# Performance work log

Measured on AMD Instinct MI355X. Metric: run time of the kernel, lower is better.

## Reference

```python
import jax, jax.numpy as jnp
import numpy as np

B, S, D, H = 4, 2048, 1024, 16
DK = D // H

def setup_inputs() -> dict:
    key = jax.random.key(0)
    ks = jax.random.split(key, 13)
    std = 1.0 / np.sqrt(D)
    inp = {
        'query': jax.random.normal(ks[0], (B, S, D), jnp.float32),
        'key':   jax.random.normal(ks[1], (B, S, D), jnp.float32),
        'value': jax.random.normal(ks[2], (B, S, D), jnp.float32),
        'mask':  jax.random.randint(ks[3], (B, 1, S), 0, 2, jnp.int32),
        'Wq': jax.random.normal(ks[4], (D, D), jnp.float32) * std,
        'bq': jnp.zeros((D,), jnp.float32),
        'Wk': jax.random.normal(ks[5], (D, D), jnp.float32) * std,
        'bk': jnp.zeros((D,), jnp.float32),
        'Wv': jax.random.normal(ks[6], (D, D), jnp.float32) * std,
        'bv': jnp.zeros((D,), jnp.float32),
        'Wo': jax.random.normal(ks[7], (D, D), jnp.float32) * std,
        'bo': jnp.zeros((D,), jnp.float32),
    }
    return inp

def reference(query, key, value, mask, Wq, bq, Wk, bk, Wv, bv, Wo, bo):
    # QKV projections (torch Linear: x @ W.T + b), reshape to [B,H,S,DK]
    def proj(x, W, b):
        y = x @ W.T + b
        return y.reshape(B, S, H, DK).transpose(0, 2, 1, 3)
    q = proj(query, Wq, bq)
    k = proj(key, Wk, bk)
    v = proj(value, Wv, bv)
    scores = jnp.einsum('bhqd,bhkd->bhqk', q, k) / jnp.sqrt(jnp.float32(DK))
    # mask [B,1,S] -> unsqueeze head dim -> [B,1,1,S], broadcast over h,q
    m = mask[:, None, :, :]  # [B,1,1,S]
    scores = jnp.where(m == 0, jnp.float32(-1e9), scores)
    p = jax.nn.softmax(scores, axis=-1)  # dropout omitted (eval mode)
    x = jnp.einsum('bhqk,bhkd->bhqd', p, v)
    x = x.transpose(0, 2, 1, 3).reshape(B, S, D)
    return x @ Wo.T + bo
```

## Files before the change

kernel.cpp:

```cpp
#include <hip/hip_runtime.h>

typedef unsigned short u16;
typedef __bf16 bf16x8 __attribute__((ext_vector_type(8)));
typedef float f32x4 __attribute__((ext_vector_type(4)));
typedef u16 u16x8 __attribute__((ext_vector_type(8)));
typedef u16 u16x4 __attribute__((ext_vector_type(4)));

typedef __attribute__((address_space(1))) const unsigned char gc_u8;
typedef __attribute__((address_space(3))) unsigned char lds_u8;

__device__ inline void gload16(const void* g, void* l) {
    __builtin_amdgcn_global_load_lds((gc_u8*)g, (lds_u8*)l, 16, 0, 0);
}
__device__ inline u16 f2bf(float f) {
    union { __bf16 h; u16 u; } c; c.h = (__bf16)f; return c.u;
}
__device__ inline float bf2f(u16 u) {
    union { u16 u[2]; float f; } c; c.u[0] = 0; c.u[1] = u; return c.f;
}
__device__ inline void hard_barrier() {
    __builtin_amdgcn_sched_barrier(0);
    __builtin_amdgcn_s_barrier();
    __builtin_amdgcn_sched_barrier(0);
}
#define WAIT_LGKM0() asm volatile("s_waitcnt lgkmcnt(0)" ::: "memory")
#define WAIT_VMCNT(n) asm volatile("s_waitcnt vmcnt(" #n ")" ::: "memory")

__global__ __launch_bounds__(256) void cvt4(const float* __restrict__ s0,
                                            const float* __restrict__ s1,
                                            const float* __restrict__ s2,
                                            const float* __restrict__ s3,
                                            u16* __restrict__ d0, u16* __restrict__ d1,
                                            u16* __restrict__ d2, u16* __restrict__ d3,
                                            int n) {
    const int y = blockIdx.y;
    const float* src = (y == 0) ? s0 : (y == 1) ? s1 : (y == 2) ? s2 : s3;
    u16* dst = (y == 0) ? d0 : (y == 1) ? d1 : (y == 2) ? d2 : d3;
    int i = (blockIdx.x * 256 + threadIdx.x) * 4;
    if (i < n) {
        float4 f = *reinterpret_cast<const float4*>(src + i);
        u16x4 u = { f2bf(f.x), f2bf(f.y), f2bf(f.z), f2bf(f.w) };
        *reinterpret_cast<u16x4*>(dst + i) = u;
    }
}
__global__ __launch_bounds__(256) void cvt3(const float* __restrict__ s0,
                                            const float* __restrict__ s1,
                                            const float* __restrict__ s2,
                                            u16* __restrict__ d0, u16* __restrict__ d1,
                                            u16* __restrict__ d2, int n) {
    const int y = blockIdx.y;
    const float* src = (y == 0) ? s0 : (y == 1) ? s1 : s2;
    u16* dst = (y == 0) ? d0 : (y == 1) ? d1 : d2;
    int i = (blockIdx.x * 256 + threadIdx.x) * 4;
    if (i < n) {
        float4 f = *reinterpret_cast<const float4*>(src + i);
        u16x4 u = { f2bf(f.x), f2bf(f.y), f2bf(f.z), f2bf(f.w) };
        *reinterpret_cast<u16x4*>(dst + i) = u;
    }
}

__global__ __launch_bounds__(256) void gemm_qkv(const u16* __restrict__ Aq,
                                                const u16* __restrict__ Ak,
                                                const u16* __restrict__ Av,
                                                const u16* __restrict__ Bq,
                                                const u16* __restrict__ Bk,
                                                const u16* __restrict__ Bv,
                                                const float* __restrict__ bq,
                                                const float* __restrict__ bk,
                                                const float* __restrict__ bv,
                                                u16* __restrict__ Cq,
                                                u16* __restrict__ Ck,
                                                u16* __restrict__ Cvp,
                                                int M, int N, int K) {
    __shared__ __align__(16) u16 As[2][128][32];
    __shared__ __align__(16) u16 Bs[2][128][32];
    const int z = blockIdx.z;
    const u16* A = (z == 0) ? Aq : (z == 1) ? Ak : Av;
    const u16* B = (z == 0) ? Bq : (z == 1) ? Bk : Bv;
    const float* bias = (z == 0) ? bq : (z == 1) ? bk : bv;
    u16* Cv = (z == 0) ? Cq : (z == 1) ? Ck : Cvp;
    const bool vmode = (z == 2);

    const int t = threadIdx.x, lane = t & 63, w = t >> 6;
    const int wr = w >> 1, wc = w & 1;
    const int l15 = lane & 15, l16 = lane >> 4;
    const int nwg = gridDim.x, ntiles = N >> 7;
    const int wg = blockIdx.x, chunk = nwg >> 3;
    const int swz = (wg & 7) * chunk + (wg >> 3);
    const int bm = (swz / ntiles) * 128, bn = (swz % ntiles) * 128;
    const int srow = w * 16 + (lane >> 2);
    const int sgr = (lane & 3) * 8;
    const u16* Ab = A + (size_t)bm * K;
    const u16* Bb = B + (size_t)bn * K;

    f32x4 acc[4][4];
#pragma unroll
    for (int i = 0; i < 4; i++)
#pragma unroll
        for (int j = 0; j < 4; j++) acc[i][j] = (f32x4){0.f, 0.f, 0.f, 0.f};

    auto stage = [&](int c, int k0) {
        gload16(Ab + (size_t)srow * K + k0 + sgr,        &As[c][w * 16][0]);
        gload16(Ab + (size_t)(64 + srow) * K + k0 + sgr, &As[c][64 + w * 16][0]);
        gload16(Bb + (size_t)srow * K + k0 + sgr,        &Bs[c][w * 16][0]);
        gload16(Bb + (size_t)(64 + srow) * K + k0 + sgr, &Bs[c][64 + w * 16][0]);
    };

    stage(0, 0);
    __syncthreads();

    const int NS = K >> 5;
    for (int i = 0; i < NS; ++i) {
        const int c = i & 1;
        WAIT_LGKM0();
        hard_barrier();
        if (i + 1 < NS) {
            stage(c ^ 1, (i + 1) * 32);
            WAIT_VMCNT(4);
        } else {
            WAIT_VMCNT(0);
        }
        hard_barrier();

        bf16x8 afr[4], bfr[4];
#pragma unroll
        for (int mi = 0; mi < 4; mi++)
            afr[mi] = *(const bf16x8*)&As[c][wr * 64 + mi * 16 + l15][l16 * 8];
#pragma unroll
        for (int ni = 0; ni < 4; ni++)
            bfr[ni] = *(const bf16x8*)&Bs[c][wc * 64 + ni * 16 + l15][l16 * 8];
#pragma unroll
        for (int mi = 0; mi < 4; mi++)
#pragma unroll
            for (int ni = 0; ni < 4; ni++)
                acc[mi][ni] = __builtin_amdgcn_mfma_f32_16x16x32_bf16(
                    afr[mi], bfr[ni], acc[mi][ni], 0, 0, 0);
    }

#pragma unroll
    for (int ni = 0; ni < 4; ni++) {
        const int col = bn + wc * 64 + ni * 16 + l15;
        const float bv2 = bias[col];
#pragma unroll
        for (int mi = 0; mi < 4; mi++) {
            const int r0 = bm + wr * 64 + mi * 16 + l16 * 4;
            if (vmode) {
                const int bb = r0 >> 11, ss = r0 & 2047;
                const int hh = col >> 6, dk = col & 63;
                u16x4 pk;
#pragma unroll
                for (int r = 0; r < 4; r++) pk[r] = f2bf(acc[mi][ni][r] + bv2);
                *(u16x4*)&Cv[(((size_t)(bb * 16 + hh) * 64 + dk) << 11) + ss] = pk;
            } else {
#pragma unroll
                for (int r = 0; r < 4; r++)
                    Cv[(size_t)(r0 + r) * N + col] = f2bf(acc[mi][ni][r] + bv2);
            }
        }
    }
}

__global__ __launch_bounds__(256) void gemm_out(const u16* __restrict__ A,
                                                const u16* __restrict__ B,
                                                const float* __restrict__ bias,
                                                float* __restrict__ Cv,
                                                int M, int N, int K) {
    __shared__ __align__(16) u16 As[2][128][32];
    __shared__ __align__(16) u16 Bs[2][128][32];
    const int t = threadIdx.x, lane = t & 63, w = t >> 6;
    const int wr = w >> 1, wc = w & 1;
    const int l15 = lane & 15, l16 = lane >> 4;
    const int nwg = gridDim.x, ntiles = N >> 7;
    const int wg = blockIdx.x, chunk = nwg >> 3;
    const int swz = (wg & 7) * chunk + (wg >> 3);
    const int bm = (swz / ntiles) * 128, bn = (swz % ntiles) * 128;
    const int srow = w * 16 + (lane >> 2);
    const int sgr = (lane & 3) * 8;
    const u16* Ab = A + (size_t)bm * K;
    const u16* Bb = B + (size_t)bn * K;

    f32x4 acc[4][4];
#pragma unroll
    for (int i = 0; i < 4; i++)
#pragma unroll
        for (int j = 0; j < 4; j++) acc[i][j] = (f32x4){0.f, 0.f, 0.f, 0.f};

    auto stage = [&](int c, int k0) {
        gload16(Ab + (size_t)srow * K + k0 + sgr,        &As[c][w * 16][0]);
        gload16(Ab + (size_t)(64 + srow) * K + k0 + sgr, &As[c][64 + w * 16][0]);
        gload16(Bb + (size_t)srow * K + k0 + sgr,        &Bs[c][w * 16][0]);
        gload16(Bb + (size_t)(64 + srow) * K + k0 + sgr, &Bs[c][64 + w * 16][0]);
    };

    stage(0, 0);
    __syncthreads();

    const int NS = K >> 5;
    for (int i = 0; i < NS; ++i) {
        const int c = i & 1;
        WAIT_LGKM0();
        hard_barrier();
        if (i + 1 < NS) {
            stage(c ^ 1, (i + 1) * 32);
            WAIT_VMCNT(4);
        } else {
            WAIT_VMCNT(0);
        }
        hard_barrier();

        bf16x8 afr[4], bfr[4];
#pragma unroll
        for (int mi = 0; mi < 4; mi++)
            afr[mi] = *(const bf16x8*)&As[c][wr * 64 + mi * 16 + l15][l16 * 8];
#pragma unroll
        for (int ni = 0; ni < 4; ni++)
            bfr[ni] = *(const bf16x8*)&Bs[c][wc * 64 + ni * 16 + l15][l16 * 8];
#pragma unroll
        for (int mi = 0; mi < 4; mi++)
#pragma unroll
            for (int ni = 0; ni < 4; ni++)
                acc[mi][ni] = __builtin_amdgcn_mfma_f32_16x16x32_bf16(
                    afr[mi], bfr[ni], acc[mi][ni], 0, 0, 0);
    }

#pragma unroll
    for (int ni = 0; ni < 4; ni++) {
        const int col = bn + wc * 64 + ni * 16 + l15;
        const float bv = bias[col];
#pragma unroll
        for (int mi = 0; mi < 4; mi++) {
            const int r0 = bm + wr * 64 + mi * 16 + l16 * 4;
#pragma unroll
            for (int r = 0; r < 4; r++)
                Cv[(size_t)(r0 + r) * N + col] = acc[mi][ni][r] + bv;
        }
    }
}

__global__ __launch_bounds__(256, 2) void attn_fwd(const u16* __restrict__ Q,
                                                   const u16* __restrict__ Kg,
                                                   const u16* __restrict__ Vt,
                                                   const int* __restrict__ mask,
                                                   u16* __restrict__ O) {
    constexpr int S = 2048, D = 1024;
    __shared__ __align__(16) u16 Kl[2][2][2][64][32];
    __shared__ __align__(16) u16 Vl[2][2][2][64][32];
    __shared__ __align__(16) u16 Pl[4][16][68];
    __shared__ unsigned Mb[64];
    const int t = threadIdx.x, lane = t & 63, w = t >> 6;
    const int l15 = lane & 15, l16 = lane >> 4;
    const int wg = blockIdx.x;
    const int swz = (wg & 7) * 64 + (wg >> 3);
    const int q0 = (swz & 7) * 256, h = (swz >> 3) & 15, b = swz >> 7;
    const int qb = q0 + w * 64;
    const int srow = w * 16 + (lane >> 2);
    const int sgr = ((lane & 3) ^ ((lane >> 3) & 3)) * 8;
    const int gsw8 = (l16 ^ ((l15 >> 1) & 3)) * 8;

    const u16* Khead = Kg + (size_t)b * S * D + h * 64;
    const u16* Vthead = Vt + (size_t)(b * 16 + h) * 64 * 2048;
    const int* mrow = mask + b * S;

    auto stage = [&](int c, int kt) {
#pragma unroll
        for (int kg = 0; kg < 2; kg++) {
            const int k0 = kt + kg * 64;
            gload16(Khead + (size_t)(k0 + srow) * D + sgr,        &Kl[c][kg][0][w * 16][0]);
            gload16(Khead + (size_t)(k0 + srow) * D + 32 + sgr,   &Kl[c][kg][1][w * 16][0]);
            gload16(Vthead + (size_t)srow * 2048 + k0 + sgr,      &Vl[c][kg][0][w * 16][0]);
            gload16(Vthead + (size_t)srow * 2048 + k0 + 32 + sgr, &Vl[c][kg][1][w * 16][0]);
        }
    };

    stage(0, 0);
#pragma unroll
    for (int j = 0; j < 8; j++) {
        unsigned long long bal = __ballot(mrow[j * 256 + w * 64 + lane] != 0);
        if (lane == 0) {
            Mb[(j * 4 + w) * 2]     = (unsigned)bal;
            Mb[(j * 4 + w) * 2 + 1] = (unsigned)(bal >> 32);
        }
    }

    constexpr float QSCALE = 0.125f * 1.44269504f;
    bf16x8 aq[4][2];
#pragma unroll
    for (int qt = 0; qt < 4; qt++)
#pragma unroll
        for (int ks = 0; ks < 2; ks++) {
            const size_t qi = ((size_t)b * S + qb + qt * 16 + l15) * D +
                              h * 64 + ks * 32 + l16 * 8;
            u16x8 raw = *(const u16x8*)&Q[qi];
            bf16x8 qv;
#pragma unroll
            for (int i = 0; i < 8; i++) qv[i] = (__bf16)(bf2f(raw[i]) * QSCALE);
            aq[qt][ks] = qv;
        }

    bf16x8 ones;
#pragma unroll
    for (int i = 0; i < 8; i++) ones[i] = (__bf16)1.0f;

    f32x4 acc[4][4];
    f32x4 accl[4];
#pragma unroll
    for (int qt = 0; qt < 4; qt++) {
        accl[qt] = (f32x4){0.f, 0.f, 0.f, 0.f};
#pragma unroll
        for (int dt = 0; dt < 4; dt++) acc[qt][dt] = (f32x4){0.f, 0.f, 0.f, 0.f};
    }

    __syncthreads();

    for (int tile = 0; tile < S / 128; ++tile) {
        const int c = tile & 1;
        const int cur = tile * 128;
        WAIT_LGKM0();
        hard_barrier();
        if (tile + 1 < S / 128) {
            stage(c ^ 1, cur + 128);
            WAIT_VMCNT(8);
        } else {
            WAIT_VMCNT(0);
        }
        hard_barrier();

#pragma unroll
        for (int kg = 0; kg < 2; kg++) {
            bf16x8 kf0[4], kf1[4], vf0[4], vf1[4];
#pragma unroll
            for (int k4 = 0; k4 < 4; k4++) {
                kf0[k4] = *(const bf16x8*)&Kl[c][kg][0][k4 * 16 + l15][gsw8];
                kf1[k4] = *(const bf16x8*)&Kl[c][kg][1][k4 * 16 + l15][gsw8];
            }
#pragma unroll
            for (int dt = 0; dt < 4; dt++) {
                vf0[dt] = *(const bf16x8*)&Vl[c][kg][0][dt * 16 + l15][gsw8];
                vf1[dt] = *(const bf16x8*)&Vl[c][kg][1][dt * 16 + l15][gsw8];
            }

            const int mb0 = (cur >> 5) + kg * 2;
            const unsigned w0 = Mb[mb0], w1 = Mb[mb0 + 1];
            float madd[4][4];
#pragma unroll
            for (int k4 = 0; k4 < 4; k4++) {
                const unsigned wsel = (k4 < 2) ? w0 : w1;
                const unsigned bits = (wsel >> ((k4 & 1) * 16 + l16 * 4)) & 0xFu;
#pragma unroll
                for (int r = 0; r < 4; r++)
                    madd[k4][r] = ((bits >> r) & 1u) ? 0.f : -1.0e9f;
            }

#pragma unroll
            for (int qt = 0; qt < 4; qt++) {
#pragma unroll
                for (int k4 = 0; k4 < 4; k4++) {
                    f32x4 z = (f32x4){0.f, 0.f, 0.f, 0.f};
                    z = __builtin_amdgcn_mfma_f32_16x16x32_bf16(kf0[k4], aq[qt][0], z, 0, 0, 0);
                    z = __builtin_amdgcn_mfma_f32_16x16x32_bf16(kf1[k4], aq[qt][1], z, 0, 0, 0);
                    u16x4 pk;
#pragma unroll
                    for (int r = 0; r < 4; r++)
                        pk[r] = f2bf(__builtin_amdgcn_exp2f(z[r] + madd[k4][r]));
                    *(u16x4*)&Pl[w][l15][k4 * 16 + l16 * 4] = pk;
                }
                bf16x8 pa0 = *(const bf16x8*)&Pl[w][l15][l16 * 8];
                bf16x8 pa1 = *(const bf16x8*)&Pl[w][l15][32 + l16 * 8];
                accl[qt] = __builtin_amdgcn_mfma_f32_16x16x32_bf16(pa0, ones, accl[qt], 0, 0, 0);
                accl[qt] = __builtin_amdgcn_mfma_f32_16x16x32_bf16(pa1, ones, accl[qt], 0, 0, 0);
#pragma unroll
                for (int dt = 0; dt < 4; dt++) {
                    acc[qt][dt] = __builtin_amdgcn_mfma_f32_16x16x32_bf16(
                        pa0, vf0[dt], acc[qt][dt], 0, 0, 0);
                    acc[qt][dt] = __builtin_amdgcn_mfma_f32_16x16x32_bf16(
                        pa1, vf1[dt], acc[qt][dt], 0, 0, 0);
                }
            }
        }
    }

#pragma unroll
    for (int qt = 0; qt < 4; qt++) {
        f32x4 inv;
#pragma unroll
        for (int r = 0; r < 4; r++) inv[r] = 1.f / accl[qt][r];
#pragma unroll
        for (int dt = 0; dt < 4; dt++)
#pragma unroll
            for (int r = 0; r < 4; r++) {
                const int tok = qb + qt * 16 + l16 * 4 + r;
                O[((size_t)b * S + tok) * D + h * 64 + dt * 16 + l15] =
                    f2bf(acc[qt][dt][r] * inv[r]);
            }
    }
}

extern "C" void kernel_launch(void* const* d_in, const int* in_sizes, int n_in,
                              void* d_out, int out_size, void* d_ws, size_t ws_size,
                              hipStream_t stream) {
    const float* query = (const float*)d_in[0];
    const float* key   = (const float*)d_in[1];
    const float* value = (const float*)d_in[2];
    const int*   mask  = (const int*)d_in[3];
    const float* Wq = (const float*)d_in[4];
    const float* bq = (const float*)d_in[5];
    const float* Wk = (const float*)d_in[6];
    const float* bk = (const float*)d_in[7];
    const float* Wv = (const float*)d_in[8];
    const float* bv = (const float*)d_in[9];
    const float* Wo = (const float*)d_in[10];
    const float* bo = (const float*)d_in[11];
    float* out = (float*)d_out;

    constexpr int S = 2048, D = 1024;
    constexpr size_t MSZ = (size_t)4 * S * D;
    constexpr size_t WSZ = (size_t)D * D;
    const size_t need = 4 * WSZ * 2 + 4 * MSZ * 2;
    if (ws_size < need) return;

    char* p = (char*)d_ws;
    u16* Wqb = (u16*)p; p += WSZ * 2;
    u16* Wkb = (u16*)p; p += WSZ * 2;
    u16* Wvb = (u16*)p; p += WSZ * 2;
    u16* Wob = (u16*)p; p += WSZ * 2;
    u16* Aq  = (u16*)p; p += MSZ * 2;
    u16* Qb  = (u16*)p; p += MSZ * 2;
    u16* Kb  = (u16*)p; p += MSZ * 2;
    u16* Vtb = (u16*)p; p += MSZ * 2;
    u16* Ak = (u16*)d_out;
    u16* Av = (u16*)d_out + MSZ;
    u16* Xb = Aq;

    cvt4<<<dim3(WSZ / 1024, 4), 256, 0, stream>>>(Wq, Wk, Wv, Wo,
                                                  Wqb, Wkb, Wvb, Wob, (int)WSZ);
    cvt3<<<dim3(MSZ / 1024, 3), 256, 0, stream>>>(query, key, value,
                                                  Aq, Ak, Av, (int)MSZ);
    gemm_qkv<<<dim3(512, 1, 3), 256, 0, stream>>>(Aq, Ak, Av, Wqb, Wkb, Wvb,
                                                  bq, bk, bv, Qb, Kb, Vtb,
                                                  8192, 1024, 1024);
    attn_fwd<<<512, 256, 0, stream>>>(Qb, Kb, Vtb, mask, Xb);
    gemm_out<<<512, 256, 0, stream>>>(Xb, Wob, bo, out, 8192, 1024, 1024);
}
```

Baseline: 206.5 us.

## Shrink attention blocks to two waves with 64-key tiles and MFMA priority hints

The attention kernel moves from 256-thread blocks covering 256 queries to 128-thread blocks covering 128 queries, launching 1024 blocks instead of 512. The key tile drops from 128 to 64 per iteration, so shared-memory buffers shrink and there are twice as many loop iterations and barriers. The QK scores for all four key sub-tiles are now computed before the exp, and s_setprio hints are placed around the MFMA sections to interleave waves. The aim is more resident blocks and better overlap, at the price of more barrier overhead and each K/V tile being reused by fewer waves.

```diff
diff --git a/kernel.cpp b/kernel.cpp
--- a/kernel.cpp
+++ b/kernel.cpp
@@ -237,21 +237,21 @@
     }
 }
 
-__global__ __launch_bounds__(256, 2) void attn_fwd(const u16* __restrict__ Q,
+__global__ __launch_bounds__(128, 2) void attn_fwd(const u16* __restrict__ Q,
                                                    const u16* __restrict__ Kg,
                                                    const u16* __restrict__ Vt,
                                                    const int* __restrict__ mask,
                                                    u16* __restrict__ O) {
     constexpr int S = 2048, D = 1024;
-    __shared__ __align__(16) u16 Kl[2][2][2][64][32];
-    __shared__ __align__(16) u16 Vl[2][2][2][64][32];
-    __shared__ __align__(16) u16 Pl[4][16][68];
+    __shared__ __align__(16) u16 Kl[2][2][64][32];
+    __shared__ __align__(16) u16 Vl[2][2][64][32];
+    __shared__ __align__(16) u16 Pl[2][16][68];
     __shared__ unsigned Mb[64];
     const int t = threadIdx.x, lane = t & 63, w = t >> 6;
     const int l15 = lane & 15, l16 = lane >> 4;
     const int wg = blockIdx.x;
-    const int swz = (wg & 7) * 64 + (wg >> 3);
-    const int q0 = (swz & 7) * 256, h = (swz >> 3) & 15, b = swz >> 7;
+    const int swz = (wg & 7) * 128 + (wg >> 3);
+    const int q0 = (swz & 15) * 128, h = (swz >> 4) & 15, b = swz >> 8;
     const int qb = q0 + w * 64;
     const int srow = w * 16 + (lane >> 2);
     const int sgr = ((lane & 3) ^ ((lane >> 3) & 3)) * 8;
@@ -262,23 +262,23 @@
     const int* mrow = mask + b * S;
 
     auto stage = [&](int c, int kt) {
-#pragma unroll
-        for (int kg = 0; kg < 2; kg++) {
-            const int k0 = kt + kg * 64;
-            gload16(Khead + (size_t)(k0 + srow) * D + sgr,        &Kl[c][kg][0][w * 16][0]);
-            gload16(Khead + (size_t)(k0 + srow) * D + 32 + sgr,   &Kl[c][kg][1][w * 16][0]);
-            gload16(Vthead + (size_t)srow * 2048 + k0 + sgr,      &Vl[c][kg][0][w * 16][0]);
-            gload16(Vthead + (size_t)srow * 2048 + k0 + 32 + sgr, &Vl[c][kg][1][w * 16][0]);
-        }
+        gload16(Khead + (size_t)(kt + srow) * D + sgr,            &Kl[c][0][w * 16][0]);
+        gload16(Khead + (size_t)(kt + 32 + srow) * D + sgr,       &Kl[c][0][32 + w * 16][0]);
+        gload16(Khead + (size_t)(kt + srow) * D + 32 + sgr,       &Kl[c][1][w * 16][0]);
+        gload16(Khead + (size_t)(kt + 32 + srow) * D + 32 + sgr,  &Kl[c][1][32 + w * 16][0]);
+        gload16(Vthead + (size_t)srow * 2048 + kt + sgr,          &Vl[c][0][w * 16][0]);
+        gload16(Vthead + (size_t)(32 + srow) * 2048 + kt + sgr,   &Vl[c][0][32 + w * 16][0]);
+        gload16(Vthead + (size_t)srow * 2048 + kt + 32 + sgr,     &Vl[c][1][w * 16][0]);
+        gload16(Vthead + (size_t)(32 + srow) * 2048 + kt + 32 + sgr, &Vl[c][1][32 + w * 16][0]);
     };
 
     stage(0, 0);
 #pragma unroll
-    for (int j = 0; j < 8; j++) {
-        unsigned long long bal = __ballot(mrow[j * 256 + w * 64 + lane] != 0);
+    for (int j = 0; j < 16; j++) {
+        unsigned long long bal = __ballot(mrow[j * 128 + w * 64 + lane] != 0);
         if (lane == 0) {
-            Mb[(j * 4 + w) * 2]     = (unsigned)bal;
-            Mb[(j * 4 + w) * 2 + 1] = (unsigned)(bal >> 32);
+            Mb[(j * 2 + w) * 2]     = (unsigned)bal;
+            Mb[(j * 2 + w) * 2 + 1] = (unsigned)(bal >> 32);
         }
     }
 
@@ -312,70 +312,74 @@
 
     __syncthreads();
 
-    for (int tile = 0; tile < S / 128; ++tile) {
+    for (int tile = 0; tile < S / 64; ++tile) {
         const int c = tile & 1;
-        const int cur = tile * 128;
+        const int cur = tile * 64;
         WAIT_LGKM0();
         hard_barrier();
-        if (tile + 1 < S / 128) {
-            stage(c ^ 1, cur + 128);
+        if (tile + 1 < S / 64) {
+            stage(c ^ 1, cur + 64);
             WAIT_VMCNT(8);
         } else {
             WAIT_VMCNT(0);
         }
         hard_barrier();
 
-#pragma unroll
-        for (int kg = 0; kg < 2; kg++) {
-            bf16x8 kf0[4], kf1[4], vf0[4], vf1[4];
+        bf16x8 kf0[4], kf1[4], vf0[4], vf1[4];
+#pragma unroll
+        for (int k4 = 0; k4 < 4; k4++) {
+            kf0[k4] = *(const bf16x8*)&Kl[c][0][k4 * 16 + l15][gsw8];
+            kf1[k4] = *(const bf16x8*)&Kl[c][1][k4 * 16 + l15][gsw8];
+        }
+#pragma unroll
+        for (int dt = 0; dt < 4; dt++) {
+            vf0[dt] = *(const bf16x8*)&Vl[c][0][dt * 16 + l15][gsw8];
+            vf1[dt] = *(const bf16x8*)&Vl[c][1][dt * 16 + l15][gsw8];
+        }
+
+        const unsigned w0 = Mb[cur >> 5], w1 = Mb[(cur >> 5) + 1];
+        float madd[4][4];
+#pragma unroll
+        for (int k4 = 0; k4 < 4; k4++) {
+            const unsigned wsel = (k4 < 2) ? w0 : w1;
+            const unsigned bits = (wsel >> ((k4 & 1) * 16 + l16 * 4)) & 0xFu;
+#pragma unroll
+            for (int r = 0; r < 4; r++)
+                madd[k4][r] = ((bits >> r) & 1u) ? 0.f : -1.0e9f;
+        }
+
+#pragma unroll
+        for (int qt = 0; qt < 4; qt++) {
+            __builtin_amdgcn_s_setprio(1);
+            f32x4 z[4];
 #pragma unroll
             for (int k4 = 0; k4 < 4; k4++) {
-                kf0[k4] = *(const bf16x8*)&Kl[c][kg][0][k4 * 16 + l15][gsw8];
-                kf1[k4] = *(const bf16x8*)&Kl[c][kg][1][k4 * 16 + l15][gsw8];
+                z[k4] = (f32x4){0.f, 0.f, 0.f, 0.f};
+                z[k4] = __builtin_amdgcn_mfma_f32_16x16x32_bf16(kf0[k4], aq[qt][0], z[k4], 0, 0, 0);
+                z[k4] = __builtin_amdgcn_mfma_f32_16x16x32_bf16(kf1[k4], aq[qt][1], z[k4], 0, 0, 0);
             }
+            __builtin_amdgcn_s_setprio(0);
+#pragma unroll
+            for (int k4 = 0; k4 < 4; k4++) {
+                u16x4 pk;
+#pragma unroll
+                for (int r = 0; r < 4; r++)
+                    pk[r] = f2bf(__builtin_amdgcn_exp2f(z[k4][r] + madd[k4][r]));
+                *(u16x4*)&Pl[w][l15][k4 * 16 + l16 * 4] = pk;
+            }
+            bf16x8 pa0 = *(const bf16x8*)&Pl[w][l15][l16 * 8];
+            bf16x8 pa1 = *(const bf16x8*)&Pl[w][l15][32 + l16 * 8];
+            __builtin_amdgcn_s_setprio(1);
+            accl[qt] = __builtin_amdgcn_mfma_f32_16x16x32_bf16(pa0, ones, accl[qt], 0, 0, 0);
+            accl[qt] = __builtin_amdgcn_mfma_f32_16x16x32_bf16(pa1, ones, accl[qt], 0, 0, 0);
 #pragma unroll
             for (int dt = 0; dt < 4; dt++) {
-                vf0[dt] = *(const bf16x8*)&Vl[c][kg][0][dt * 16 + l15][gsw8];
-                vf1[dt] = *(const bf16x8*)&Vl[c][kg][1][dt * 16 + l15][gsw8];
+                acc[qt][dt] = __builtin_amdgcn_mfma_f32_16x16x32_bf16(
+                    pa0, vf0[dt], acc[qt][dt], 0, 0, 0);
+                acc[qt][dt] = __builtin_amdgcn_mfma_f32_16x16x32_bf16(
+                    pa1, vf1[dt], acc[qt][dt], 0, 0, 0);
             }
-
-            const int mb0 = (cur >> 5) + kg * 2;
-            const unsigned w0 = Mb[mb0], w1 = Mb[mb0 + 1];
-            float madd[4][4];
-#pragma unroll
-            for (int k4 = 0; k4 < 4; k4++) {
-                const unsigned wsel = (k4 < 2) ? w0 : w1;
-                const unsigned bits = (wsel >> ((k4 & 1) * 16 + l16 * 4)) & 0xFu;
-#pragma unroll
-                for (int r = 0; r < 4; r++)
-                    madd[k4][r] = ((bits >> r) & 1u) ? 0.f : -1.0e9f;
-            }
-
-#pragma unroll
-            for (int qt = 0; qt < 4; qt++) {
-#pragma unroll
-                for (int k4 = 0; k4 < 4; k4++) {
-                    f32x4 z = (f32x4){0.f, 0.f, 0.f, 0.f};
-                    z = __builtin_amdgcn_mfma_f32_16x16x32_bf16(kf0[k4], aq[qt][0], z, 0, 0, 0);
-                    z = __builtin_amdgcn_mfma_f32_16x16x32_bf16(kf1[k4], aq[qt][1], z, 0, 0, 0);
-                    u16x4 pk;
-#pragma unroll
-                    for (int r = 0; r < 4; r++)
-                        pk[r] = f2bf(__builtin_amdgcn_exp2f(z[r] + madd[k4][r]));
-                    *(u16x4*)&Pl[w][l15][k4 * 16 + l16 * 4] = pk;
-                }
-                bf16x8 pa0 = *(const bf16x8*)&Pl[w][l15][l16 * 8];
-                bf16x8 pa1 = *(const bf16x8*)&Pl[w][l15][32 + l16 * 8];
-                accl[qt] = __builtin_amdgcn_mfma_f32_16x16x32_bf16(pa0, ones, accl[qt], 0, 0, 0);
-                accl[qt] = __builtin_amdgcn_mfma_f32_16x16x32_bf16(pa1, ones, accl[qt], 0, 0, 0);
-#pragma unroll
-                for (int dt = 0; dt < 4; dt++) {
-                    acc[qt][dt] = __builtin_amdgcn_mfma_f32_16x16x32_bf16(
-                        pa0, vf0[dt], acc[qt][dt], 0, 0, 0);
-                    acc[qt][dt] = __builtin_amdgcn_mfma_f32_16x16x32_bf16(
-                        pa1, vf1[dt], acc[qt][dt], 0, 0, 0);
-                }
-            }
+            __builtin_amdgcn_s_setprio(0);
         }
     }
 
@@ -438,6 +442,6 @@
     gemm_qkv<<<dim3(512, 1, 3), 256, 0, stream>>>(Aq, Ak, Av, Wqb, Wkb, Wvb,
                                                   bq, bk, bv, Qb, Kb, Vtb,
                                                   8192, 1024, 1024);
-    attn_fwd<<<512, 256, 0, stream>>>(Qb, Kb, Vtb, mask, Xb);
+    attn_fwd<<<1024, 128, 0, stream>>>(Qb, Kb, Vtb, mask, Xb);
     gemm_out<<<512, 256, 0, stream>>>(Xb, Wob, bo, out, 8192, 1024, 1024);
 }
```

Result: slower. 213.5 us (+3.3%).

## Fuse fp32-to-bf16 activation conversion into QKV GEMM operand loading

Applied to the files above, without the earlier changes.

Removes the separate cvt3 kernel that converted query/key/value to bf16. The QKV GEMM now streams fp32 activations directly into LDS with an XOR-swizzled layout and converts them to bf16 when building MFMA fragments. This avoids writing and re-reading bf16 copies of three large activation tensors and drops one kernel launch. In exchange, the GEMM reads twice as many A-operand bytes per tile, uses twice the LDS for A, and does conversion work in the inner loop, which is repeated across the N-tiles that share the same A rows.

```diff
diff --git a/kernel.cpp b/kernel.cpp
--- a/kernel.cpp
+++ b/kernel.cpp
@@ -43,25 +43,10 @@
         *reinterpret_cast<u16x4*>(dst + i) = u;
     }
 }
-__global__ __launch_bounds__(256) void cvt3(const float* __restrict__ s0,
-                                            const float* __restrict__ s1,
-                                            const float* __restrict__ s2,
-                                            u16* __restrict__ d0, u16* __restrict__ d1,
-                                            u16* __restrict__ d2, int n) {
-    const int y = blockIdx.y;
-    const float* src = (y == 0) ? s0 : (y == 1) ? s1 : s2;
-    u16* dst = (y == 0) ? d0 : (y == 1) ? d1 : d2;
-    int i = (blockIdx.x * 256 + threadIdx.x) * 4;
-    if (i < n) {
-        float4 f = *reinterpret_cast<const float4*>(src + i);
-        u16x4 u = { f2bf(f.x), f2bf(f.y), f2bf(f.z), f2bf(f.w) };
-        *reinterpret_cast<u16x4*>(dst + i) = u;
-    }
-}
-
-__global__ __launch_bounds__(256) void gemm_qkv(const u16* __restrict__ Aq,
-                                                const u16* __restrict__ Ak,
-                                                const u16* __restrict__ Av,
+
+__global__ __launch_bounds__(256) void gemm_qkv(const float* __restrict__ Aq,
+                                                const float* __restrict__ Ak,
+                                                const float* __restrict__ Av,
                                                 const u16* __restrict__ Bq,
                                                 const u16* __restrict__ Bk,
                                                 const u16* __restrict__ Bv,
@@ -72,10 +57,10 @@
                                                 u16* __restrict__ Ck,
                                                 u16* __restrict__ Cvp,
                                                 int M, int N, int K) {
-    __shared__ __align__(16) u16 As[2][128][32];
+    __shared__ __align__(16) float Asf[2][128][32];
     __shared__ __align__(16) u16 Bs[2][128][32];
     const int z = blockIdx.z;
-    const u16* A = (z == 0) ? Aq : (z == 1) ? Ak : Av;
+    const float* A = (z == 0) ? Aq : (z == 1) ? Ak : Av;
     const u16* B = (z == 0) ? Bq : (z == 1) ? Bk : Bv;
     const float* bias = (z == 0) ? bq : (z == 1) ? bk : bv;
     u16* Cv = (z == 0) ? Cq : (z == 1) ? Ck : Cvp;
@@ -90,7 +75,8 @@
     const int bm = (swz / ntiles) * 128, bn = (swz % ntiles) * 128;
     const int srow = w * 16 + (lane >> 2);
     const int sgr = (lane & 3) * 8;
-    const u16* Ab = A + (size_t)bm * K;
+    const int arsub = lane >> 3;
+    const int agr = ((lane & 7) ^ (lane >> 3)) * 4;
     const u16* Bb = B + (size_t)bn * K;
 
     f32x4 acc[4][4];
@@ -100,8 +86,10 @@
         for (int j = 0; j < 4; j++) acc[i][j] = (f32x4){0.f, 0.f, 0.f, 0.f};
 
     auto stage = [&](int c, int k0) {
-        gload16(Ab + (size_t)srow * K + k0 + sgr,        &As[c][w * 16][0]);
-        gload16(Ab + (size_t)(64 + srow) * K + k0 + sgr, &As[c][64 + w * 16][0]);
+#pragma unroll
+        for (int ch = 0; ch < 4; ch++)
+            gload16(A + (size_t)(bm + ch * 32 + w * 8 + arsub) * K + k0 + agr,
+                    &Asf[c][ch * 32 + w * 8][0]);
         gload16(Bb + (size_t)srow * K + k0 + sgr,        &Bs[c][w * 16][0]);
         gload16(Bb + (size_t)(64 + srow) * K + k0 + sgr, &Bs[c][64 + w * 16][0]);
     };
@@ -116,16 +104,26 @@
         hard_barrier();
         if (i + 1 < NS) {
             stage(c ^ 1, (i + 1) * 32);
-            WAIT_VMCNT(4);
+            WAIT_VMCNT(6);
         } else {
             WAIT_VMCNT(0);
         }
         hard_barrier();
 
+        const int key = l15 & 7;
         bf16x8 afr[4], bfr[4];
 #pragma unroll
-        for (int mi = 0; mi < 4; mi++)
-            afr[mi] = *(const bf16x8*)&As[c][wr * 64 + mi * 16 + l15][l16 * 8];
+        for (int mi = 0; mi < 4; mi++) {
+            const int rr = wr * 64 + mi * 16 + l15;
+            f32x4 lo = *(const f32x4*)&Asf[c][rr][((2 * l16) ^ key) * 4];
+            f32x4 hi = *(const f32x4*)&Asf[c][rr][((2 * l16 + 1) ^ key) * 4];
+            bf16x8 v;
+            v[0] = (__bf16)lo[0]; v[1] = (__bf16)lo[1];
+            v[2] = (__bf16)lo[2]; v[3] = (__bf16)lo[3];
+            v[4] = (__bf16)hi[0]; v[5] = (__bf16)hi[1];
+            v[6] = (__bf16)hi[2]; v[7] = (__bf16)hi[3];
+            afr[mi] = v;
+        }
 #pragma unroll
         for (int ni = 0; ni < 4; ni++)
             bfr[ni] = *(const bf16x8*)&Bs[c][wc * 64 + ni * 16 + l15][l16 * 8];
@@ -423,21 +421,16 @@
     u16* Wkb = (u16*)p; p += WSZ * 2;
     u16* Wvb = (u16*)p; p += WSZ * 2;
     u16* Wob = (u16*)p; p += WSZ * 2;
-    u16* Aq  = (u16*)p; p += MSZ * 2;
+    u16* Xb  = (u16*)p; p += MSZ * 2;
     u16* Qb  = (u16*)p; p += MSZ * 2;
     u16* Kb  = (u16*)p; p += MSZ * 2;
     u16* Vtb = (u16*)p; p += MSZ * 2;
-    u16* Ak = (u16*)d_out;
-    u16* Av = (u16*)d_out + MSZ;
-    u16* Xb = Aq;
 
     cvt4<<<dim3(WSZ / 1024, 4), 256, 0, stream>>>(Wq, Wk, Wv, Wo,
                                                   Wqb, Wkb, Wvb, Wob, (int)WSZ);
-    cvt3<<<dim3(MSZ / 1024, 3), 256, 0, stream>>>(query, key, value,
-                                                  Aq, Ak, Av, (int)MSZ);
-    gemm_qkv<<<dim3(512, 1, 3), 256, 0, stream>>>(Aq, Ak, Av, Wqb, Wkb, Wvb,
-                                                  bq, bk, bv, Qb, Kb, Vtb,
-                                                  8192, 1024, 1024);
+    gemm_qkv<<<dim3(512, 1, 3), 256, 0, stream>>>(query, key, value,
+                                                  Wqb, Wkb, Wvb, bq, bk, bv,
+                                                  Qb, Kb, Vtb, 8192, 1024, 1024);
     attn_fwd<<<512, 256, 0, stream>>>(Qb, Kb, Vtb, mask, Xb);
     gemm_out<<<512, 256, 0, stream>>>(Xb, Wob, bo, out, 8192, 1024, 1024);
 }
```

Result: faster. 192.1 us (-7.0%).
